# Kernel optimization log

Hardware: AMD Instinct MI355X
Metric: run time of the kernel (lower is better)

## Reference

```python
import jax, jax.numpy as jnp
import numpy as np
from jax import lax

INSZ, HSZ, NLAYERS = 1024, 1024, 2
B, T = 32, 512
FORGET_BIAS = 1.0


def setup_inputs() -> dict:
    key = jax.random.key(0)
    ks = jax.random.split(key, 6)
    x = jax.random.normal(ks[0], (B, T, INSZ), dtype=jnp.float32)
    lengths = jax.random.randint(ks[1], (B,), 1, T + 1, dtype=jnp.int32)
    s0 = 1.0 / np.sqrt(INSZ + HSZ)
    s1 = 1.0 / np.sqrt(HSZ + HSZ)
    W0 = jax.random.uniform(ks[2], (INSZ + HSZ, 4 * HSZ), jnp.float32, -s0, s0)
    b0 = jnp.zeros((4 * HSZ,), jnp.float32)
    W1 = jax.random.uniform(ks[3], (HSZ + HSZ, 4 * HSZ), jnp.float32, -s1, s1)
    b1 = jnp.zeros((4 * HSZ,), jnp.float32)
    return {"x": x, "lengths": lengths, "W0": W0, "b0": b0, "W1": W1, "b1": b1}


def _lstm_layer(x, lengths, W, b):
    # x: [B, T, D_in]; TF LSTMCell gate order (i, j, f, o), forget_bias added to f.
    bsz = x.shape[0]
    hsz = b.shape[0] // 4
    tsteps = jnp.arange(x.shape[1])

    def step(carry, inp):
        h, c = carry
        xt, t = inp
        z = jnp.concatenate([xt, h], axis=-1) @ W + b  # [B, 4H]
        i, j, f, o = jnp.split(z, 4, axis=-1)
        c_new = jax.nn.sigmoid(f + FORGET_BIAS) * c + jax.nn.sigmoid(i) * jnp.tanh(j)
        h_new = jax.nn.sigmoid(o) * jnp.tanh(c_new)
        mask = (t < lengths)[:, None]
        # dynamic_rnn: zero outputs past sequence_length, freeze state
        h_out = jnp.where(mask, h_new, 0.0)
        h_keep = jnp.where(mask, h_new, h)
        c_keep = jnp.where(mask, c_new, c)
        return (h_keep, c_keep), h_out

    init = (jnp.zeros((bsz, hsz), x.dtype), jnp.zeros((bsz, hsz), x.dtype))
    (h_fin, c_fin), ys = lax.scan(step, init, (jnp.swapaxes(x, 0, 1), tsteps))
    return jnp.swapaxes(ys, 0, 1), h_fin, c_fin


def reference(x, lengths, W0, b0, W1, b1):
    out0, _, _ = _lstm_layer(x, lengths, W0, b0)
    out1, h1, c1 = _lstm_layer(out0, lengths, W1, b1)
    return out1, (h1, c1)
```

## Files before the change

### kernel.cpp

```cpp
#include <hip/hip_runtime.h>
#include <hip/hip_bf16.h>

typedef unsigned short u16;
typedef unsigned int u32;
typedef unsigned long long u64;
typedef short s8v __attribute__((ext_vector_type(8)));
typedef float f4v __attribute__((ext_vector_type(4)));

#define BQ 32
#define TQ 512
#define DQ 1024
#define CHUNK 128
#define NCHUNK (TQ / CHUNK)
#define NTHR 256
#define NBLK_R 256

__device__ __host__ inline u16 f2bf(float f) {
    union { float f; unsigned u; } v; v.f = f;
    unsigned r = v.u + 0x7fffu + ((v.u >> 16) & 1u);
    return (u16)(r >> 16);
}
__device__ __host__ inline float bf2f(u16 u) {
    union { unsigned u; float f; } v; v.u = ((unsigned)u) << 16;
    return v.f;
}
__device__ inline u32 packsplit(float f) {
    u16 hi = f2bf(f);
    u16 lo = f2bf(f - bf2f(hi));
    return ((u32)hi << 16) | (u32)lo;
}

__global__ void init_kernel(u32* __restrict__ z0, size_t n0,
                            u32* __restrict__ z1, size_t n1) {
    size_t i = (size_t)blockIdx.x * blockDim.x + threadIdx.x;
    size_t stride = (size_t)gridDim.x * blockDim.x;
    for (size_t idx = i; idx < n0; idx += stride) z0[idx] = 0;
    for (size_t idx = i; idx < n1; idx += stride) z1[idx] = 0;
}

__global__ void pack_w_kernel(const float* __restrict__ W, u32* __restrict__ wpkT) {
    size_t i = (size_t)blockIdx.x * blockDim.x + threadIdx.x;
    size_t stride = (size_t)gridDim.x * blockDim.x;
    const size_t NTOT = (size_t)4 * DQ * DQ;
    for (size_t idx = i; idx < NTOT; idx += stride) {
        size_t n = idx >> 10, k = idx & 1023;
        wpkT[idx] = packsplit(W[k * (4 * DQ) + n]);
    }
}

__global__ void pack_x_kernel(const float* __restrict__ x, u32* __restrict__ xpk,
                              int t0) {
    size_t i = (size_t)blockIdx.x * blockDim.x + threadIdx.x;
    size_t stride = (size_t)gridDim.x * blockDim.x;
    const size_t NTOT = (size_t)BQ * CHUNK * DQ;
    for (size_t idx = i; idx < NTOT; idx += stride) {
        size_t b = idx >> 17;
        size_t r = idx & 131071;
        size_t tl = r >> 10, k = r & 1023;
        xpk[idx] = packsplit(x[((size_t)b * TQ + t0 + tl) * DQ + k]);
    }
}

__device__ inline void unpack_pk(uint4 A, uint4 B, s8v& hi, s8v& lo) {
    union { u32 u[4]; s8v v; } H, L;
    H.u[0] = (A.x >> 16) | (A.y & 0xffff0000u); L.u[0] = (A.x & 0xffffu) | (A.y << 16);
    H.u[1] = (A.z >> 16) | (A.w & 0xffff0000u); L.u[1] = (A.z & 0xffffu) | (A.w << 16);
    H.u[2] = (B.x >> 16) | (B.y & 0xffff0000u); L.u[2] = (B.x & 0xffffu) | (B.y << 16);
    H.u[3] = (B.z >> 16) | (B.w & 0xffff0000u); L.u[3] = (B.z & 0xffffu) | (B.w << 16);
    hi = H.v; lo = L.v;
}

__global__ __launch_bounds__(NTHR) void xproj_gemm_kernel(
    const u32* __restrict__ apk,
    const int* __restrict__ lens,
    const u32* __restrict__ wpkT,
    const float* __restrict__ bias,
    float* __restrict__ zx,
    int t0, int is_l1)
{
    __shared__ u32 Asp[128][36];
    __shared__ u32 Bsp[128][36];

    const int tid = threadIdx.x;
    const int bm = blockIdx.x & 31;
    const int bn = blockIdx.x >> 5;

    const int wv = tid >> 6;
    const int wm = wv >> 1, wn = wv & 1;
    const int lane = tid & 63;
    const int frow = lane & 15;
    const int quad = lane >> 4;

    const int am = tid >> 1;
    const int akh = (tid & 1) * 16;
    const int amg = bm * 128 + am;
    const int ab = amg >> 7;
    const int atl = amg & 127;
    const int at = t0 + atl;

    bool arow_live = true;
    size_t arow;
    if (!is_l1) {
        arow = (size_t)amg * DQ;
    } else {
        arow = ((size_t)(at + 1) * BQ + ab) * DQ;
        arow_live = (at < lens[ab]);
    }
    const u32* bbase = wpkT + (size_t)(bn * 128 + am) * DQ;

    f4v acc[4][4];
    #pragma unroll
    for (int i = 0; i < 4; ++i)
        #pragma unroll
        for (int j = 0; j < 4; ++j) acc[i][j] = (f4v){0.f, 0.f, 0.f, 0.f};

    for (int kt = 0; kt < 32; ++kt) {
        const int k0 = kt * 32;
        {
            const u32* src = apk + arow + k0 + akh;
            #pragma unroll
            for (int j4 = 0; j4 < 4; ++j4) {
                uint4 v = ((const uint4*)src)[j4];
                if (!arow_live) { v.x = v.y = v.z = v.w = 0; }
                *(uint4*)&Asp[am][akh + 4 * j4] = v;
            }
        }
        {
            const u32* src = bbase + k0 + akh;
            #pragma unroll
            for (int j4 = 0; j4 < 4; ++j4) {
                uint4 v = ((const uint4*)src)[j4];
                *(uint4*)&Bsp[am][akh + 4 * j4] = v;
            }
        }
        __syncthreads();

        s8v ah[4], al[4], bh[4], bl[4];
        #pragma unroll
        for (int mt = 0; mt < 4; ++mt) {
            uint4 a0 = *(const uint4*)&Asp[wm * 64 + mt * 16 + frow][quad * 8];
            uint4 a1 = *(const uint4*)&Asp[wm * 64 + mt * 16 + frow][quad * 8 + 4];
            unpack_pk(a0, a1, ah[mt], al[mt]);
        }
        #pragma unroll
        for (int nt = 0; nt < 4; ++nt) {
            uint4 b0 = *(const uint4*)&Bsp[wn * 64 + nt * 16 + frow][quad * 8];
            uint4 b1 = *(const uint4*)&Bsp[wn * 64 + nt * 16 + frow][quad * 8 + 4];
            unpack_pk(b0, b1, bh[nt], bl[nt]);
        }
        #pragma unroll
        for (int mt = 0; mt < 4; ++mt)
            #pragma unroll
            for (int nt = 0; nt < 4; ++nt) {
                acc[mt][nt] = __builtin_amdgcn_mfma_f32_16x16x32_bf16(ah[mt], bh[nt], acc[mt][nt], 0, 0, 0);
                acc[mt][nt] = __builtin_amdgcn_mfma_f32_16x16x32_bf16(al[mt], bh[nt], acc[mt][nt], 0, 0, 0);
                acc[mt][nt] = __builtin_amdgcn_mfma_f32_16x16x32_bf16(ah[mt], bl[nt], acc[mt][nt], 0, 0, 0);
            }
        __syncthreads();
    }

    float bv[4];
    #pragma unroll
    for (int nt = 0; nt < 4; ++nt) bv[nt] = bias[bn * 128 + wn * 64 + nt * 16 + frow];
    #pragma unroll
    for (int mt = 0; mt < 4; ++mt) {
        #pragma unroll
        for (int nt = 0; nt < 4; ++nt) {
            int col = bn * 128 + wn * 64 + nt * 16 + frow;
            #pragma unroll
            for (int r = 0; r < 4; ++r) {
                int row = bm * 128 + wm * 64 + mt * 16 + quad * 4 + r;
                zx[(size_t)row * (4 * DQ) + col] = acc[mt][nt][r] + bv[nt];
            }
        }
    }
}

__global__ __launch_bounds__(NTHR, 1) void lstm_rec_kernel(
    const float* __restrict__ zx,
    const float* __restrict__ W,
    const int* __restrict__ lens,
    u32* __restrict__ hh,
    u32* __restrict__ subc,
    u32* __restrict__ topc,
    float* __restrict__ state_h,
    float* __restrict__ state_c,
    float* __restrict__ out_f32,
    float* __restrict__ hc_out,
    int t0, int is_last)
{
    __shared__ u16 wt[2][32][1032];
    __shared__ float red[4][16][36];

    const int tid = threadIdx.x;
    const int blk = blockIdx.x;
    const int bg = blk & 1;
    const int cg = blk >> 1;
    const int grp = (blk >> 1) & 7;

    for (int idx = tid; idx < 32 * 1024; idx += NTHR) {
        int n = idx & 31, k = idx >> 5;
        int c = n >> 2, g = n & 3;
        float w = W[(size_t)(DQ + k) * (4 * DQ) + g * DQ + cg * 8 + c];
        u16 wh = f2bf(w);
        wt[0][n][k] = wh;
        wt[1][n][k] = f2bf(w - bf2f(wh));
    }

    const int gb_l = tid >> 3;
    const int gc = tid & 7;
    const int b_g = bg * 16 + gb_l;
    const int hcol = cg * 8 + gc;
    float c_state = 0.f, h_state = 0.f;
    int mylen = 0;
    if (tid < 128) {
        mylen = lens[b_g];
        h_state = state_h[(size_t)b_g * DQ + hcol];
        c_state = state_c[(size_t)b_g * DQ + hcol];
    }

    const int wave = tid >> 6;
    const int lane = tid & 63;
    const int frow = lane & 15;
    const int quad = lane >> 4;
    const int ksrc = wave * 256;

    __syncthreads();

    const int tend = t0 + CHUNK;
    for (int t = t0; t < tend; ++t) {
        const u32* hp = hh + ((size_t)t * BQ + (bg * 16 + frow)) * DQ + ksrc + quad * 8;
        uint4 q[16];
        #pragma unroll
        for (int s = 0; s < 8; ++s) {
            q[2 * s]     = ((const uint4*)(hp + s * 32))[0];
            q[2 * s + 1] = ((const uint4*)(hp + s * 32))[1];
        }

        f4v acc0 = {0.f, 0.f, 0.f, 0.f};
        f4v acc1 = {0.f, 0.f, 0.f, 0.f};
        #pragma unroll
        for (int s = 0; s < 8; ++s) {
            s8v a_h, a_l;
            unpack_pk(q[2 * s], q[2 * s + 1], a_h, a_l);
            const int koff = ksrc + s * 32 + quad * 8;
            s8v b0h = *(const s8v*)&wt[0][frow][koff];
            s8v b0l = *(const s8v*)&wt[1][frow][koff];
            s8v b1h = *(const s8v*)&wt[0][16 + frow][koff];
            s8v b1l = *(const s8v*)&wt[1][16 + frow][koff];
            acc0 = __builtin_amdgcn_mfma_f32_16x16x32_bf16(a_h, b0h, acc0, 0, 0, 0);
            acc1 = __builtin_amdgcn_mfma_f32_16x16x32_bf16(a_h, b1h, acc1, 0, 0, 0);
            acc0 = __builtin_amdgcn_mfma_f32_16x16x32_bf16(a_l, b0h, acc0, 0, 0, 0);
            acc1 = __builtin_amdgcn_mfma_f32_16x16x32_bf16(a_l, b1h, acc1, 0, 0, 0);
            acc0 = __builtin_amdgcn_mfma_f32_16x16x32_bf16(a_h, b0l, acc0, 0, 0, 0);
            acc1 = __builtin_amdgcn_mfma_f32_16x16x32_bf16(a_h, b1l, acc1, 0, 0, 0);
        }
        #pragma unroll
        for (int r = 0; r < 4; ++r) {
            red[wave][quad * 4 + r][frow] = acc0[r];
            red[wave][quad * 4 + r][16 + frow] = acc1[r];
        }

        float zxv[4];
        if (tid < 128) {
            size_t base = ((size_t)b_g * CHUNK + (t - t0)) * (4 * DQ) + hcol;
            #pragma unroll
            for (int g = 0; g < 4; ++g) zxv[g] = zx[base + (size_t)g * DQ];
        }
        __syncthreads();

        if (tid < 128) {
            float z[4];
            #pragma unroll
            for (int g = 0; g < 4; ++g) {
                int n = gc * 4 + g;
                z[g] = red[0][gb_l][n] + red[1][gb_l][n] + red[2][gb_l][n] + red[3][gb_l][n]
                     + zxv[g];
            }
            float si = 1.f / (1.f + __expf(-z[0]));
            float sf = 1.f / (1.f + __expf(-(z[2] + 1.0f)));
            float so = 1.f / (1.f + __expf(-z[3]));
            float cn = sf * c_state + si * tanhf(z[1]);
            float hn = so * tanhf(cn);
            bool m = (t < mylen);
            float hk = m ? hn : h_state;
            float ck = m ? cn : c_state;
            h_state = hk; c_state = ck;

            u16 hh16 = f2bf(hk);
            u16 hl16 = f2bf(hk - bf2f(hh16));
            u32 packed = ((u32)hh16 << 16) | (u32)hl16;
            __hip_atomic_store(hh + ((size_t)(t + 1) * BQ + b_g) * DQ + hcol,
                               packed, __ATOMIC_RELAXED, __HIP_MEMORY_SCOPE_AGENT);

            if (is_last) {
                float ho = m ? hn : 0.f;
                out_f32[((size_t)b_g * TQ + t) * DQ + hcol] = ho;
            }
        }

        asm volatile("s_waitcnt vmcnt(0)" ::: "memory");
        __syncthreads();
        if (t < tend - 1) {
            if (tid == 0) {
                u32* sc = &subc[((t * 2 + bg) * 8 + grp) * 16];
                u32* tc = &topc[(t * 2 + bg) * 16];
                u32 old = atomicAdd(sc, 1u);
                if (old == 15) atomicAdd(tc, 1u);
                while (__hip_atomic_load(tc, __ATOMIC_RELAXED,
                                         __HIP_MEMORY_SCOPE_AGENT) < 8) { }
            }
            __syncthreads();
        }
    }

    if (tid < 128) {
        state_h[(size_t)b_g * DQ + hcol] = h_state;
        state_c[(size_t)b_g * DQ + hcol] = c_state;
        if (is_last && tend == TQ) {
            hc_out[(size_t)b_g * DQ + hcol] = h_state;
            hc_out[(size_t)BQ * DQ + (size_t)b_g * DQ + hcol] = c_state;
        }
    }
}

extern "C" void kernel_launch(void* const* d_in, const int* in_sizes, int n_in,
                              void* d_out, int out_size, void* d_ws, size_t ws_size,
                              hipStream_t stream) {
    const float* x    = (const float*)d_in[0];
    const int*   lens = (const int*)d_in[1];
    const float* W0   = (const float*)d_in[2];
    const float* b0   = (const float*)d_in[3];
    const float* W1   = (const float*)d_in[4];
    const float* b1   = (const float*)d_in[5];
    float* out = (float*)d_out;

    const size_t N   = (size_t)BQ * TQ * DQ;
    const size_t ZXN = (size_t)BQ * CHUNK * 4 * DQ;
    const size_t HD  = (size_t)BQ * DQ;
    const size_t WPK = (size_t)4 * DQ * DQ;
    const size_t XPK = (size_t)BQ * CHUNK * DQ;

    float* zx  = (float*)d_ws;
    u32* hh    = (u32*)(zx + ZXN);
    float* sh0 = (float*)(hh + (size_t)(TQ + 1) * HD);
    float* sc0 = sh0 + HD;
    float* sh1 = sc0 + HD;
    float* sc1 = sh1 + HD;
    u32* sub0  = (u32*)(sc1 + HD);
    u32* top0  = sub0 + (size_t)TQ * 2 * 8 * 16;
    u32* sub1  = top0 + (size_t)TQ * 2 * 16;
    u32* top1  = sub1 + (size_t)TQ * 2 * 8 * 16;
    u32* zend  = top1 + (size_t)TQ * 2 * 16;
    const size_t nzero = (size_t)(zend - (u32*)sh0);
    u32* wpk0  = zend;
    u32* wpk1  = wpk0 + WPK;
    u32* xpk   = wpk1 + WPK;

    init_kernel<<<256, 256, 0, stream>>>(hh, HD, (u32*)sh0, nzero);
    pack_w_kernel<<<2048, 256, 0, stream>>>(W0, wpk0);
    pack_w_kernel<<<2048, 256, 0, stream>>>(W1, wpk1);

    for (int c = 0; c < NCHUNK; ++c) {
        int t0 = c * CHUNK;
        pack_x_kernel<<<2048, 256, 0, stream>>>(x, xpk, t0);
        xproj_gemm_kernel<<<1024, NTHR, 0, stream>>>(xpk, lens, wpk0, b0, zx, t0, 0);
        lstm_rec_kernel<<<NBLK_R, NTHR, 0, stream>>>(
            zx, W0, lens, hh, sub0, top0, sh0, sc0,
            nullptr, nullptr, t0, 0);
    }
    for (int c = 0; c < NCHUNK; ++c) {
        int t0 = c * CHUNK;
        xproj_gemm_kernel<<<1024, NTHR, 0, stream>>>(hh, lens, wpk1, b1, zx, t0, 1);
        lstm_rec_kernel<<<NBLK_R, NTHR, 0, stream>>>(
            zx, W1, lens, hh, sub1, top1, sh1, sc1,
            out, out + N, t0, 1);
    }
}
```

Before: 6.965 ms.

## Replace hierarchical atomic grid barrier with per-block ready flags polled per wave

Each recurrent timestep used to end with a two-level atomic counter barrier: one thread per block increments counters and spins until all blocks of its batch group arrive. Now each block just stores a ready flag for its column slice after writing h. At the start of the next step, each wave polls, with cache-bypassing loads, only the 32 flags covering the K range it reads. This removes atomic RMW contention and replaces the full barrier with dependency-driven waiting, which should shorten the per-step synchronisation latency on the serial path. The cost is more polling loads per wave, and correctness now depends on visibility ordering between the relaxed h stores and the flag store.

```diff
diff --git a/kernel.cpp b/kernel.cpp
--- a/kernel.cpp
+++ b/kernel.cpp
@@ -181,8 +181,7 @@
     const float* __restrict__ W,
     const int* __restrict__ lens,
     u32* __restrict__ hh,
-    u32* __restrict__ subc,
-    u32* __restrict__ topc,
+    u32* __restrict__ sent,
     float* __restrict__ state_h,
     float* __restrict__ state_c,
     float* __restrict__ out_f32,
@@ -196,7 +195,6 @@
     const int blk = blockIdx.x;
     const int bg = blk & 1;
     const int cg = blk >> 1;
-    const int grp = (blk >> 1) & 7;
 
     for (int idx = tid; idx < 32 * 1024; idx += NTHR) {
         int n = idx & 31, k = idx >> 5;
@@ -229,6 +227,18 @@
 
     const int tend = t0 + CHUNK;
     for (int t = t0; t < tend; ++t) {
+        if (t > t0) {
+            const u32* fp = sent + ((size_t)(t - 1) * 2 + bg) * 128
+                          + wave * 32 + (lane & 31);
+            u32 f;
+            do {
+                asm volatile("global_load_dword %0, %1, off sc0 sc1"
+                             : "=v"(f) : "v"(fp));
+                asm volatile("s_waitcnt vmcnt(0)" ::: "memory");
+            } while (__any(f == 0u));
+            __builtin_amdgcn_sched_barrier(0);
+        }
+
         const u32* hp = hh + ((size_t)t * BQ + (bg * 16 + frow)) * DQ + ksrc + quad * 8;
         uint4 q[16];
         #pragma unroll
@@ -301,17 +311,9 @@
 
         asm volatile("s_waitcnt vmcnt(0)" ::: "memory");
         __syncthreads();
-        if (t < tend - 1) {
-            if (tid == 0) {
-                u32* sc = &subc[((t * 2 + bg) * 8 + grp) * 16];
-                u32* tc = &topc[(t * 2 + bg) * 16];
-                u32 old = atomicAdd(sc, 1u);
-                if (old == 15) atomicAdd(tc, 1u);
-                while (__hip_atomic_load(tc, __ATOMIC_RELAXED,
-                                         __HIP_MEMORY_SCOPE_AGENT) < 8) { }
-            }
-            __syncthreads();
-        }
+        if (tid == 0 && t < tend - 1)
+            __hip_atomic_store(sent + ((size_t)t * 2 + bg) * 128 + cg, 1u,
+                               __ATOMIC_RELAXED, __HIP_MEMORY_SCOPE_AGENT);
     }
 
     if (tid < 128) {
@@ -339,7 +341,7 @@
     const size_t ZXN = (size_t)BQ * CHUNK * 4 * DQ;
     const size_t HD  = (size_t)BQ * DQ;
     const size_t WPK = (size_t)4 * DQ * DQ;
-    const size_t XPK = (size_t)BQ * CHUNK * DQ;
+    const size_t SEN = (size_t)TQ * 2 * 128;
 
     float* zx  = (float*)d_ws;
     u32* hh    = (u32*)(zx + ZXN);
@@ -347,11 +349,9 @@
     float* sc0 = sh0 + HD;
     float* sh1 = sc0 + HD;
     float* sc1 = sh1 + HD;
-    u32* sub0  = (u32*)(sc1 + HD);
-    u32* top0  = sub0 + (size_t)TQ * 2 * 8 * 16;
-    u32* sub1  = top0 + (size_t)TQ * 2 * 16;
-    u32* top1  = sub1 + (size_t)TQ * 2 * 8 * 16;
-    u32* zend  = top1 + (size_t)TQ * 2 * 16;
+    u32* sen0  = (u32*)(sc1 + HD);
+    u32* sen1  = sen0 + SEN;
+    u32* zend  = sen1 + SEN;
     const size_t nzero = (size_t)(zend - (u32*)sh0);
     u32* wpk0  = zend;
     u32* wpk1  = wpk0 + WPK;
@@ -366,14 +366,14 @@
         pack_x_kernel<<<2048, 256, 0, stream>>>(x, xpk, t0);
         xproj_gemm_kernel<<<1024, NTHR, 0, stream>>>(xpk, lens, wpk0, b0, zx, t0, 0);
         lstm_rec_kernel<<<NBLK_R, NTHR, 0, stream>>>(
-            zx, W0, lens, hh, sub0, top0, sh0, sc0,
+            zx, W0, lens, hh, sen0, sh0, sc0,
             nullptr, nullptr, t0, 0);
     }
     for (int c = 0; c < NCHUNK; ++c) {
         int t0 = c * CHUNK;
         xproj_gemm_kernel<<<1024, NTHR, 0, stream>>>(hh, lens, wpk1, b1, zx, t0, 1);
         lstm_rec_kernel<<<NBLK_R, NTHR, 0, stream>>>(
-            zx, W1, lens, hh, sub1, top1, sh1, sc1,
+            zx, W1, lens, hh, sen1, sh1, sc1,
             out, out + N, t0, 1);
     }
 }
```

Result: slower. 7.521 ms (+8.0%).
